# Kernel optimization log

Measured on AMD Instinct MI355X. Metric: run time of the kernel, lower is better.

The kernel has to match this reference:

```python
import jax, jax.numpy as jnp
import numpy as np

D_MODEL = 1024
SEL_DIM = 64
CONFIGS = [(4, 32), (8, 64), (16, 128)]  # (heads, dim)
B, T = 2, 2048


def setup_inputs() -> dict:
    key = jax.random.key(0)
    ks = jax.random.split(key, 20)
    s = 0.02  # init scale for stability
    inp = {
        "x": jax.random.normal(ks[0], (B, T, D_MODEL), jnp.float32),
        "sel_w1": jax.random.normal(ks[1], (SEL_DIM, D_MODEL), jnp.float32) * s,
        "sel_b1": jnp.zeros((SEL_DIM,), jnp.float32),
        "sel_w2": jax.random.normal(ks[2], (SEL_DIM, SEL_DIM), jnp.float32) * s,
        "sel_b2": jnp.zeros((SEL_DIM,), jnp.float32),
        "sel_w3": jax.random.normal(ks[3], (len(CONFIGS), SEL_DIM), jnp.float32) * s,
        "sel_b3": jnp.zeros((len(CONFIGS),), jnp.float32),
    }
    for i, (h, d) in enumerate(CONFIGS):
        inp[f"qw{i}"] = jax.random.normal(ks[4 + 3 * i], (h * d, D_MODEL), jnp.float32) * s
        inp[f"kw{i}"] = jax.random.normal(ks[5 + 3 * i], (d, D_MODEL), jnp.float32) * s
        inp[f"ww{i}"] = jax.random.normal(ks[6 + 3 * i], (h, D_MODEL), jnp.float32) * s
    return inp


def _seq_features(x):
    # x: [b,t,d]
    b, t, d = x.shape
    seq_mean = jnp.mean(x, axis=1, keepdims=True)            # [b,1,d]
    seq_std = jnp.std(x, axis=1, keepdims=True, ddof=1)      # torch.std is unbiased
    pos = (jnp.arange(t, dtype=x.dtype) / t)[None, :, None]  # [1,t,1] broadcast to [b,t,d]
    return x + seq_mean + seq_std + pos * 0.1


def _forward(x, sel_w1, sel_b1, sel_w2, sel_b2, sel_w3, sel_b3,
             qw0, kw0, ww0, qw1, kw1, ww1, qw2, kw2, ww2):
    b, t, dm = x.shape
    feats = _seq_features(x)
    h1 = jax.nn.relu(feats @ sel_w1.T + sel_b1)
    h2 = jax.nn.relu(h1 @ sel_w2.T + sel_b2)
    config_probs = jax.nn.softmax(h2 @ sel_w3.T + sel_b3, axis=-1)  # [b,t,ncfg]

    per_cfg = [(qw0, kw0, ww0), (qw1, kw1, ww1), (qw2, kw2, ww2)]
    final = jnp.zeros((b, t, t), dtype=x.dtype)
    for i, ((heads, dim), (qw, kw, ww)) in enumerate(zip(CONFIGS, per_cfg)):
        q = (x @ qw.T).reshape(b, t, heads, dim)   # [b,t,h,d]
        k = x @ kw.T                               # [b,s,d]
        w = x @ ww.T                               # [b,t,h]
        dots = jnp.einsum('bthd,bsd->bths', q, k)  # [b,t,h,s]
        score = jnp.einsum('bths,bth->bts', jax.nn.relu(dots), w)  # relu*weight, sum heads
        final = final + config_probs[:, :, i:i + 1] * score
    return final


def reference(x, sel_w1, sel_b1, sel_w2, sel_b2, sel_w3, sel_b3,
              qw0, kw0, ww0, qw1, kw1, ww1, qw2, kw2, ww2):
    return _forward(x, sel_w1, sel_b1, sel_w2, sel_b2, sel_w3, sel_b3,
                    qw0, kw0, ww0, qw1, kw1, ww1, qw2, kw2, ww2)
```

## Files before the change

### kernel.cpp

```cpp
#include <hip/hip_runtime.h>
#include <hip/hip_fp16.h>
#include <cstdint>
#include <cstddef>
#include <math.h>

#define B_ 2
#define T_ 2048
#define D_ 1024
#define M_ (B_*T_)

#define QO0 0
#define KO0 128
#define WO0 160
#define QO1 168
#define KO1 680
#define WO1 744
#define QO2 752
#define KO2 2800
#define WO2 2928
#define SELO 2944
#define LDN 3072

typedef float f32x16 __attribute__((ext_vector_type(16)));
typedef short bf16x8 __attribute__((ext_vector_type(8)));
typedef unsigned short u16;

__device__ __forceinline__ u16 f2bf(float f) {
    unsigned int u = __float_as_uint(f);
    unsigned int r = (u + 0x7fffu + ((u >> 16) & 1u)) >> 16;
    return (u16)r;
}
__device__ __forceinline__ float bf2f(u16 b) {
    return __uint_as_float(((unsigned int)b) << 16);
}

__device__ __forceinline__ void gload16(const void* g, void* l) {
    __builtin_amdgcn_global_load_lds(
        (const __attribute__((address_space(1))) unsigned int*)g,
        (__attribute__((address_space(3))) unsigned int*)l,
        16, 0, 0);
}

__device__ __forceinline__ void stage_plane(const u16* src_base, int row_stride, int k0,
                                            int rg, int lane, u16* dst) {
    int rl  = lane >> 2;
    int row = rg * 16 + rl;
    int q   = (lane & 3) ^ (rl & 3) ^ ((rl >> 2) & 3);
    const u16* s = src_base + (size_t)row * row_stride + k0 + q * 8;
    gload16(s, dst + rg * 512);
}

__global__ void stats1(const float* __restrict__ x, float* __restrict__ part,
                       float* __restrict__ part2, u16* __restrict__ Xh) {
    int d  = blockIdx.x * 256 + threadIdx.x;
    int tc = blockIdx.y;
    int b  = blockIdx.z;
    size_t base = (size_t)b * T_ * D_ + (size_t)tc * 64 * D_ + d;
    float s = 0.f, s2 = 0.f;
#pragma unroll 8
    for (int t = 0; t < 64; ++t) {
        float v = x[base + (size_t)t * D_];
        s += v; s2 += v * v;
        Xh[base + (size_t)t * D_] = f2bf(v);
    }
    part [(b * 32 + tc) * D_ + d] = s;
    part2[(b * 32 + tc) * D_ + d] = s2;
}

__global__ void stats2(const float* __restrict__ part, const float* __restrict__ part2,
                       const float* __restrict__ w1,
                       float* __restrict__ msd, float* __restrict__ s1) {
    __shared__ float msL[1024];
    __shared__ float ps[64][17];
    __shared__ float pw[64][17];
    int b = blockIdx.x, tid = threadIdx.x;
    float s = 0.f, s2 = 0.f;
#pragma unroll 8
    for (int i = 0; i < 32; ++i) {
        s  += part [(b * 32 + i) * D_ + tid];
        s2 += part2[(b * 32 + i) * D_ + tid];
    }
    float mean = s / (float)T_;
    float var  = (s2 - (float)T_ * mean * mean) / (float)(T_ - 1);
    msL[tid] = mean + sqrtf(fmaxf(var, 0.f));
    __syncthreads();
    int j = tid >> 4, cc = tid & 15;
    float am = 0.f, aw = 0.f;
    const float* wr = w1 + (size_t)j * D_ + cc * 64;
    const float* mr = msL + cc * 64;
    for (int dd = 0; dd < 64; ++dd) { float w = wr[dd]; am += mr[dd] * w; aw += w; }
    ps[j][cc] = am; pw[j][cc] = aw;
    __syncthreads();
    if (tid < 64) {
        float sm = 0.f, sw = 0.f;
        for (int i = 0; i < 16; ++i) { sm += ps[tid][i]; sw += pw[tid][i]; }
        msd[b * 64 + tid] = sm;
        if (b == 0) s1[tid] = sw;
    }
}

__global__ void split_w(const float* __restrict__ qw0, const float* __restrict__ kw0,
                        const float* __restrict__ ww0, const float* __restrict__ qw1,
                        const float* __restrict__ kw1, const float* __restrict__ ww1,
                        const float* __restrict__ qw2, const float* __restrict__ kw2,
                        const float* __restrict__ ww2, const float* __restrict__ w1s,
                        u16* __restrict__ Wh) {
    int row = blockIdx.x;
    int col = threadIdx.x * 4;
    const float* src = nullptr;
    if      (row < 128)  src = qw0 + (size_t)row * D_;
    else if (row < 160)  src = kw0 + (size_t)(row - 128) * D_;
    else if (row < 164)  src = ww0 + (size_t)(row - 160) * D_;
    else if (row < 168)  src = nullptr;
    else if (row < 680)  src = qw1 + (size_t)(row - 168) * D_;
    else if (row < 744)  src = kw1 + (size_t)(row - 680) * D_;
    else if (row < 752)  src = ww1 + (size_t)(row - 744) * D_;
    else if (row < 2800) src = qw2 + (size_t)(row - 752) * D_;
    else if (row < 2928) src = kw2 + (size_t)(row - 2800) * D_;
    else if (row < 2944) src = ww2 + (size_t)(row - 2928) * D_;
    else if (row < 3008) src = w1s + (size_t)(row - 2944) * D_;
    float4 v = src ? *(const float4*)(src + col) : make_float4(0.f, 0.f, 0.f, 0.f);
    ushort4 h;
    h.x = f2bf(v.x); h.y = f2bf(v.y); h.z = f2bf(v.z); h.w = f2bf(v.w);
    *(ushort4*)&Wh[(size_t)row * D_ + col] = h;
}

__global__ __launch_bounds__(256, 3) void proj_gemm(
    const u16* __restrict__ Xh, const u16* __restrict__ Wh, u16* __restrict__ Ph) {
    __shared__ u16 As[8192], Bs[8192];
    int tid = threadIdx.x;
    int wave = tid >> 6, lane = tid & 63;
    int bm = blockIdx.x * 128, bn = blockIdx.y * 128;
    int wt = wave >> 1, wn = wave & 1;
    int fm = lane & 31, hv = lane >> 5;
    int tkey = (fm & 3) ^ ((fm >> 2) & 3);
    f32x16 acc[2][2];
#pragma unroll
    for (int i = 0; i < 2; ++i)
#pragma unroll
        for (int j = 0; j < 2; ++j)
#pragma unroll
            for (int r = 0; r < 16; ++r) acc[i][j][r] = 0.f;

    const u16* xh = Xh + (size_t)bm * D_;
    const u16* wh = Wh + (size_t)bn * D_;

    for (int kc = 0; kc < 16; ++kc) {
        int k0 = kc * 64;
#pragma unroll
        for (int i = 0; i < 8; ++i) {
            int j = wave * 8 + i;
            int mat = j >> 4;
            int pl  = (j >> 3) & 1;
            int rg  = j & 7;
            stage_plane(mat ? wh : xh, D_, k0 + pl * 32, rg, lane,
                        (mat ? Bs : As) + pl * 4096);
        }
        __syncthreads();
#pragma unroll
        for (int ks = 0; ks < 4; ++ks) {
            int pl = ks >> 1;
            int slot8 = (((ks & 1) * 2 + hv) ^ tkey) * 8;
            bf16x8 a_h[2], b_h[2];
#pragma unroll
            for (int t = 0; t < 2; ++t) {
                a_h[t] = *(const bf16x8*)&As[pl * 4096 + (wt * 64 + t * 32 + fm) * 32 + slot8];
                b_h[t] = *(const bf16x8*)&Bs[pl * 4096 + (wn * 64 + t * 32 + fm) * 32 + slot8];
            }
#pragma unroll
            for (int ti = 0; ti < 2; ++ti)
#pragma unroll
                for (int tj = 0; tj < 2; ++tj)
                    acc[ti][tj] = __builtin_amdgcn_mfma_f32_32x32x16_bf16(a_h[ti], b_h[tj], acc[ti][tj], 0, 0, 0);
        }
        __syncthreads();
    }
#pragma unroll
    for (int ti = 0; ti < 2; ++ti)
#pragma unroll
        for (int tj = 0; tj < 2; ++tj)
#pragma unroll
            for (int r = 0; r < 16; ++r) {
                int row = bm + wt * 64 + ti * 32 + (r & 3) + 8 * (r >> 2) + 4 * hv;
                int col = bn + wn * 64 + tj * 32 + fm;
                Ph[(size_t)row * LDN + col] = f2bf(acc[ti][tj][r]);
            }
}

__global__ void selector2(const u16* __restrict__ Ph,
                          const float* __restrict__ msd, const float* __restrict__ s1,
                          const float* __restrict__ b1, const float* __restrict__ w2,
                          const float* __restrict__ b2, const float* __restrict__ w3,
                          const float* __restrict__ b3, __half* __restrict__ WP) {
    __shared__ float h1s[4][64];
    __shared__ float h2s[4][64];
    __shared__ float lg[4][3];
    int tid = threadIdx.x;
    int slot = tid >> 6, j = tid & 63;
    int bt = blockIdx.x * 4 + slot;
    int b = bt >> 11, t = bt & 2047;
    size_t pidx = (size_t)bt * LDN + SELO + j;
    float v = bf2f(Ph[pidx])
            + msd[b * 64 + j] + 0.1f * ((float)t / (float)T_) * s1[j] + b1[j];
    h1s[slot][j] = fmaxf(v, 0.f);
    __syncthreads();
    float a2 = b2[j];
#pragma unroll 8
    for (int d = 0; d < 64; ++d) a2 = fmaf(h1s[slot][d], w2[j * 64 + d], a2);
    h2s[slot][j] = fmaxf(a2, 0.f);
    __syncthreads();
    if (j < 3) {
        float a3 = b3[j];
        for (int d = 0; d < 64; ++d) a3 = fmaf(h2s[slot][d], w3[j * 64 + d], a3);
        lg[slot][j] = a3;
    }
    __syncthreads();
    if (j < 28) {
        float m = fmaxf(lg[slot][0], fmaxf(lg[slot][1], lg[slot][2]));
        float e0 = expf(lg[slot][0] - m), e1 = expf(lg[slot][1] - m), e2 = expf(lg[slot][2] - m);
        float inv = 1.f / (e0 + e1 + e2);
        int wcol = (j < 4) ? (WO0 + j) : ((j < 12) ? (WO1 + j - 4) : (WO2 + j - 12));
        float p = ((j < 4) ? e0 : ((j < 12) ? e1 : e2)) * inv;
        float w = bf2f(Ph[(size_t)bt * LDN + wcol]);
        WP[(size_t)(b * 28 + j) * T_ + t] = __float2half(w * p);
    }
}

__device__ __forceinline__ int qcol_of(int c) {
    if (c < 2)  return QO0 + c * 64;
    if (c < 10) return QO1 + (c - 2) * 64;
    return QO2 + (c - 10) * 64;
}

__global__ __launch_bounds__(256, 2) void score_kernel(
    const u16* __restrict__ Ph, const __half* __restrict__ WP, float* __restrict__ out) {
    __shared__ u16 Qs[2][8192];
    __shared__ u16 Ks[4 * 4096];
    __shared__ __half wpL[3584];
    int tid = threadIdx.x;
    int wave = tid >> 6, lane = tid & 63;
    int wt = wave >> 1, wn = wave & 1;
    int fm = lane & 31, hv = lane >> 5;
    int tkey = (fm & 3) ^ ((fm >> 2) & 3);

    int n = blockIdx.z * 256 + blockIdx.y * 16 + blockIdx.x;
    int p = (n & 7) * 4 + (n >> 7);
    int xb = (n >> 3) & 15;
    int b = p >> 4, yb = p & 15;
    int t0 = yb * 128, s0 = xb * 128;

    const u16* Pq = Ph + (size_t)(b * T_ + t0) * LDN;
    const u16* Pk = Ph + (size_t)(b * T_ + s0) * LDN;

    auto stageQ = [&](int buf, int qcol) {
#pragma unroll
        for (int i = 0; i < 4; ++i) {
            int j = (wave << 2) + i;
            int pl = j >> 3, rg = j & 7;
            stage_plane(Pq, LDN, qcol + pl * 32, rg, lane, &Qs[buf][pl * 4096]);
        }
    };

#pragma unroll
    for (int i = 0; i < 6; ++i) {
        int j = i * 4 + wave;
        int pl = j >> 3, rg = j & 7;
        int col = (pl == 0) ? KO0 : ((pl == 1) ? KO1 : KO1 + 32);
        stage_plane(Pk, LDN, col, rg, lane, &Ks[pl * 4096]);
    }
#pragma unroll
    for (int i = 0; i < 2; ++i) {
        int j = i * 4 + wave;
        if (j < 7) {
            const __half* src = WP + (size_t)(b * 28 + j * 4 + (lane >> 4)) * T_ + t0 + (lane & 15) * 8;
            gload16(src, (u16*)wpL + j * 512);
        }
    }
    stageQ(0, QO0);

    f32x16 outacc[2][2], dots[2][2], Z16;
#pragma unroll
    for (int r = 0; r < 16; ++r) Z16[r] = 0.f;
#pragma unroll
    for (int i = 0; i < 2; ++i)
#pragma unroll
        for (int j = 0; j < 2; ++j)
#pragma unroll
            for (int r = 0; r < 16; ++r) { outacc[i][j][r] = 0.f; dots[i][j][r] = 0.f; }

    auto epi = [&](int g) {
#pragma unroll
        for (int ti = 0; ti < 2; ++ti) {
            int rowbase = wt * 64 + ti * 32 + 4 * hv;
#pragma unroll
            for (int rq = 0; rq < 4; ++rq) {
                const __half2* wp2 = (const __half2*)&wpL[g * 128 + rowbase + rq * 8];
                float2 f01 = __half22float2(wp2[0]);
                float2 f23 = __half22float2(wp2[1]);
                float wv[4] = {f01.x, f01.y, f23.x, f23.y};
#pragma unroll
                for (int tj = 0; tj < 2; ++tj)
#pragma unroll
                    for (int r2 = 0; r2 < 4; ++r2) {
                        int r = rq * 4 + r2;
                        outacc[ti][tj][r] += fmaxf(dots[ti][tj][r], 0.f) * wv[r2];
                    }
            }
        }
    };

    auto runPhase = [&](int c, int kpA, int kpB, bool z0, bool midBreak,
                        int gMid, bool hasEnd, int gEnd) {
        if (c + 1 < 42) {
            stageQ((c + 1) & 1, qcol_of(c + 1));
            asm volatile("s_waitcnt vmcnt(4)" ::: "memory");
        } else {
            asm volatile("s_waitcnt vmcnt(0)" ::: "memory");
        }
        __builtin_amdgcn_s_barrier();
        __builtin_amdgcn_sched_barrier(0);
        const u16* qb = Qs[c & 1];

        bf16x8 kf[2][2], qf[2][2];
        auto loadks = [&](int ks, int sl) {
            int kp = (ks < 2) ? kpA : kpB;
            int slot8 = (((ks & 1) * 2 + hv) ^ tkey) * 8;
#pragma unroll
            for (int tj = 0; tj < 2; ++tj)
                kf[sl][tj] = *(const bf16x8*)&Ks[kp * 4096 + (wn * 64 + tj * 32 + fm) * 32 + slot8];
#pragma unroll
            for (int ti = 0; ti < 2; ++ti)
                qf[sl][ti] = *(const bf16x8*)&qb[(ks >> 1) * 4096 + (wt * 64 + ti * 32 + fm) * 32 + slot8];
        };
        loadks(0, 0);
#pragma unroll
        for (int ks = 0; ks < 4; ++ks) {
            if (ks < 3) loadks(ks + 1, (ks + 1) & 1);
            bool zero = (ks == 0 && z0) || (ks == 2 && midBreak);
            int sl = ks & 1;
            __builtin_amdgcn_s_setprio(1);
#pragma unroll
            for (int ti = 0; ti < 2; ++ti)
#pragma unroll
                for (int tj = 0; tj < 2; ++tj)
                    dots[ti][tj] = __builtin_amdgcn_mfma_f32_32x32x16_bf16(
                        qf[sl][ti], kf[sl][tj], zero ? Z16 : dots[ti][tj], 0, 0, 0);
            __builtin_amdgcn_s_setprio(0);
            if (ks == 1 && midBreak) epi(gMid);
            if (ks == 3 && hasEnd)   epi(gEnd);
        }
        __builtin_amdgcn_sched_barrier(0);
        __builtin_amdgcn_s_barrier();
    };

#pragma unroll
    for (int c = 0; c < 2; ++c)
        runPhase(c, 0, 0, true, true, 2 * c, true, 2 * c + 1);
    for (int h = 0; h < 8; ++h) {
        runPhase(2 + h, 1, 2, true, false, -1, true, 4 + h);
        if (h == 7) {
            for (int j = wave; j < 32; j += 4) {
                int pl = j >> 3, rg = j & 7;
                stage_plane(Pk, LDN, KO2 + pl * 32, rg, lane, &Ks[pl * 4096]);
            }
        }
    }
    for (int h = 0; h < 16; ++h) {
        runPhase(10 + 2 * h, 0, 1, true, false, -1, false, -1);
        runPhase(11 + 2 * h, 2, 3, false, false, -1, true, 12 + h);
    }

#pragma unroll
    for (int ti = 0; ti < 2; ++ti)
#pragma unroll
        for (int tj = 0; tj < 2; ++tj)
#pragma unroll
            for (int r = 0; r < 16; ++r) {
                int trow = wt * 64 + ti * 32 + (r & 3) + 8 * (r >> 2) + 4 * hv;
                int scol = wn * 64 + tj * 32 + fm;
                out[(size_t)(b * T_ + t0 + trow) * T_ + (s0 + scol)] = outacc[ti][tj][r];
            }
}

extern "C" void kernel_launch(void* const* d_in, const int* in_sizes, int n_in,
                              void* d_out, int out_size, void* d_ws, size_t ws_size,
                              hipStream_t stream) {
    const float* x   = (const float*)d_in[0];
    const float* w1  = (const float*)d_in[1];
    const float* b1  = (const float*)d_in[2];
    const float* w2  = (const float*)d_in[3];
    const float* b2  = (const float*)d_in[4];
    const float* w3  = (const float*)d_in[5];
    const float* b3  = (const float*)d_in[6];
    const float* qw0 = (const float*)d_in[7];
    const float* kw0 = (const float*)d_in[8];
    const float* ww0 = (const float*)d_in[9];
    const float* qw1 = (const float*)d_in[10];
    const float* kw1 = (const float*)d_in[11];
    const float* ww1 = (const float*)d_in[12];
    const float* qw2 = (const float*)d_in[13];
    const float* kw2 = (const float*)d_in[14];
    const float* ww2 = (const float*)d_in[15];
    float* out = (float*)d_out;

    float* fb = (float*)d_ws;
    float* PA  = fb; fb += (size_t)B_ * 32 * D_;
    float* PA2 = fb; fb += (size_t)B_ * 32 * D_;
    float* MSD = fb; fb += 128;
    float* S1  = fb; fb += 64;
    __half* WP = (__half*)fb; fb += (size_t)B_ * 28 * T_ / 2;
    u16* ub = (u16*)fb;
    u16* Wh = ub; ub += (size_t)LDN * D_;
    u16* Xh = ub; ub += (size_t)M_ * D_;
    u16* Ph = ub; ub += (size_t)M_ * LDN;

    stats1<<<dim3(D_ / 256, 32, B_), 256, 0, stream>>>(x, PA, PA2, Xh);
    stats2<<<dim3(B_), 1024, 0, stream>>>(PA, PA2, w1, MSD, S1);
    split_w<<<dim3(LDN), 256, 0, stream>>>(qw0, kw0, ww0, qw1, kw1, ww1,
                                           qw2, kw2, ww2, w1, Wh);
    proj_gemm<<<dim3(M_ / 128, LDN / 128), 256, 0, stream>>>(Xh, Wh, Ph);
    selector2<<<dim3(M_ / 4), 256, 0, stream>>>(Ph, MSD, S1, b1, w2, b2, w3, b3, WP);
    score_kernel<<<dim3(T_ / 128, T_ / 128, B_), 256, 0, stream>>>(Ph, WP, out);
}
```

Before: 250.6 us.

## Load Q fragments directly from global memory instead of double-buffered LDS staging

Removes the double-buffered shared-memory staging of Q tiles and the per-phase barriers. Each wave now loads its Q MFMA fragments straight from global memory (L2-resident projections) into registers, while K stays in LDS and is restaged with explicit barriers only between config groups. This cuts LDS traffic, LDS footprint and block-wide synchronisation. In exchange, global load latency sits directly in front of the MFMAs with no software prefetch, and each wave issues uncoalesced row-strided loads.

```diff
diff --git a/kernel.cpp b/kernel.cpp
--- a/kernel.cpp
+++ b/kernel.cpp
@@ -226,15 +226,8 @@
     }
 }
 
-__device__ __forceinline__ int qcol_of(int c) {
-    if (c < 2)  return QO0 + c * 64;
-    if (c < 10) return QO1 + (c - 2) * 64;
-    return QO2 + (c - 10) * 64;
-}
-
 __global__ __launch_bounds__(256, 2) void score_kernel(
     const u16* __restrict__ Ph, const __half* __restrict__ WP, float* __restrict__ out) {
-    __shared__ u16 Qs[2][8192];
     __shared__ u16 Ks[4 * 4096];
     __shared__ __half wpL[3584];
     int tid = threadIdx.x;
@@ -252,15 +245,6 @@
     const u16* Pq = Ph + (size_t)(b * T_ + t0) * LDN;
     const u16* Pk = Ph + (size_t)(b * T_ + s0) * LDN;
 
-    auto stageQ = [&](int buf, int qcol) {
-#pragma unroll
-        for (int i = 0; i < 4; ++i) {
-            int j = (wave << 2) + i;
-            int pl = j >> 3, rg = j & 7;
-            stage_plane(Pq, LDN, qcol + pl * 32, rg, lane, &Qs[buf][pl * 4096]);
-        }
-    };
-
 #pragma unroll
     for (int i = 0; i < 6; ++i) {
         int j = i * 4 + wave;
@@ -276,7 +260,9 @@
             gload16(src, (u16*)wpL + j * 512);
         }
     }
-    stageQ(0, QO0);
+    asm volatile("s_waitcnt vmcnt(0)" ::: "memory");
+    __builtin_amdgcn_s_barrier();
+    __builtin_amdgcn_sched_barrier(0);
 
     f32x16 outacc[2][2], dots[2][2], Z16;
 #pragma unroll
@@ -309,65 +295,59 @@
         }
     };
 
-    auto runPhase = [&](int c, int kpA, int kpB, bool z0, bool midBreak,
+    auto runPhase = [&](int qcol, int kpA, int kpB, bool z0, bool midBreak,
                         int gMid, bool hasEnd, int gEnd) {
-        if (c + 1 < 42) {
-            stageQ((c + 1) & 1, qcol_of(c + 1));
-            asm volatile("s_waitcnt vmcnt(4)" ::: "memory");
-        } else {
-            asm volatile("s_waitcnt vmcnt(0)" ::: "memory");
-        }
-        __builtin_amdgcn_s_barrier();
-        __builtin_amdgcn_sched_barrier(0);
-        const u16* qb = Qs[c & 1];
-
-        bf16x8 kf[2][2], qf[2][2];
-        auto loadks = [&](int ks, int sl) {
+        const u16* q0 = Pq + (size_t)(wt * 64 + fm) * LDN + qcol + hv * 8;
+        const u16* q1 = q0 + (size_t)32 * LDN;
+        bf16x8 qf[2][4];
+#pragma unroll
+        for (int ks = 0; ks < 4; ++ks) {
+            qf[0][ks] = *(const bf16x8*)(q0 + ks * 16);
+            qf[1][ks] = *(const bf16x8*)(q1 + ks * 16);
+        }
+#pragma unroll
+        for (int ks = 0; ks < 4; ++ks) {
             int kp = (ks < 2) ? kpA : kpB;
             int slot8 = (((ks & 1) * 2 + hv) ^ tkey) * 8;
+            bf16x8 kf[2];
 #pragma unroll
             for (int tj = 0; tj < 2; ++tj)
-                kf[sl][tj] = *(const bf16x8*)&Ks[kp * 4096 + (wn * 64 + tj * 32 + fm) * 32 + slot8];
-#pragma unroll
-            for (int ti = 0; ti < 2; ++ti)
-                qf[sl][ti] = *(const bf16x8*)&qb[(ks >> 1) * 4096 + (wt * 64 + ti * 32 + fm) * 32 + slot8];
-        };
-        loadks(0, 0);
-#pragma unroll
-        for (int ks = 0; ks < 4; ++ks) {
-            if (ks < 3) loadks(ks + 1, (ks + 1) & 1);
+                kf[tj] = *(const bf16x8*)&Ks[kp * 4096 + (wn * 64 + tj * 32 + fm) * 32 + slot8];
             bool zero = (ks == 0 && z0) || (ks == 2 && midBreak);
-            int sl = ks & 1;
             __builtin_amdgcn_s_setprio(1);
 #pragma unroll
             for (int ti = 0; ti < 2; ++ti)
 #pragma unroll
                 for (int tj = 0; tj < 2; ++tj)
                     dots[ti][tj] = __builtin_amdgcn_mfma_f32_32x32x16_bf16(
-                        qf[sl][ti], kf[sl][tj], zero ? Z16 : dots[ti][tj], 0, 0, 0);
+                        qf[ti][ks], kf[tj], zero ? Z16 : dots[ti][tj], 0, 0, 0);
             __builtin_amdgcn_s_setprio(0);
             if (ks == 1 && midBreak) epi(gMid);
             if (ks == 3 && hasEnd)   epi(gEnd);
         }
-        __builtin_amdgcn_sched_barrier(0);
-        __builtin_amdgcn_s_barrier();
     };
 
 #pragma unroll
     for (int c = 0; c < 2; ++c)
-        runPhase(c, 0, 0, true, true, 2 * c, true, 2 * c + 1);
-    for (int h = 0; h < 8; ++h) {
-        runPhase(2 + h, 1, 2, true, false, -1, true, 4 + h);
-        if (h == 7) {
-            for (int j = wave; j < 32; j += 4) {
-                int pl = j >> 3, rg = j & 7;
-                stage_plane(Pk, LDN, KO2 + pl * 32, rg, lane, &Ks[pl * 4096]);
-            }
-        }
-    }
+        runPhase(QO0 + c * 64, 0, 0, true, true, 2 * c, true, 2 * c + 1);
+    for (int h = 0; h < 8; ++h)
+        runPhase(QO1 + h * 64, 1, 2, true, false, -1, true, 4 + h);
+
+    __builtin_amdgcn_sched_barrier(0);
+    asm volatile("s_waitcnt lgkmcnt(0)" ::: "memory");
+    __builtin_amdgcn_s_barrier();
+    __builtin_amdgcn_sched_barrier(0);
+    for (int j = wave; j < 32; j += 4) {
+        int pl = j >> 3, rg = j & 7;
+        stage_plane(Pk, LDN, KO2 + pl * 32, rg, lane, &Ks[pl * 4096]);
+    }
+    asm volatile("s_waitcnt vmcnt(0)" ::: "memory");
+    __builtin_amdgcn_s_barrier();
+    __builtin_amdgcn_sched_barrier(0);
+
     for (int h = 0; h < 16; ++h) {
-        runPhase(10 + 2 * h, 0, 1, true, false, -1, false, -1);
-        runPhase(11 + 2 * h, 2, 3, false, false, -1, true, 12 + h);
+        runPhase(QO2 + (2 * h) * 64,     0, 1, true,  false, -1, false, -1);
+        runPhase(QO2 + (2 * h + 1) * 64, 2, 3, false, false, -1, true, 12 + h);
     }
 
 #pragma unroll
```

Result: slower. 266.7 us (+6.4%).

## Split score kernel tiles across eight waves instead of four

Applied to the files above, without the earlier changes.

The score kernel goes from 256 to 512 threads per block. Each wave now owns a 64x32 output sub-tile instead of 64x64, and staging of Q, K and WP is spread over eight waves. The K/Q fragment double-buffering is removed in favour of simple per-step loads, and an explicit wait and barrier are added after the initial staging. This is meant to raise latency hiding and occupancy through more waves with fewer accumulator registers each, at the cost of more LDS reads per MFMA and more barrier participants.

```diff
diff --git a/kernel.cpp b/kernel.cpp
--- a/kernel.cpp
+++ b/kernel.cpp
@@ -232,14 +232,14 @@
     return QO2 + (c - 10) * 64;
 }
 
-__global__ __launch_bounds__(256, 2) void score_kernel(
+__global__ __launch_bounds__(512, 4) void score_kernel(
     const u16* __restrict__ Ph, const __half* __restrict__ WP, float* __restrict__ out) {
     __shared__ u16 Qs[2][8192];
     __shared__ u16 Ks[4 * 4096];
     __shared__ __half wpL[3584];
     int tid = threadIdx.x;
     int wave = tid >> 6, lane = tid & 63;
-    int wt = wave >> 1, wn = wave & 1;
+    int wt = wave >> 2, wn = wave & 3;
     int fm = lane & 31, hv = lane >> 5;
     int tkey = (fm & 3) ^ ((fm >> 2) & 3);
 
@@ -254,39 +254,34 @@
 
     auto stageQ = [&](int buf, int qcol) {
 #pragma unroll
-        for (int i = 0; i < 4; ++i) {
-            int j = (wave << 2) + i;
+        for (int i = 0; i < 2; ++i) {
+            int j = wave * 2 + i;
             int pl = j >> 3, rg = j & 7;
             stage_plane(Pq, LDN, qcol + pl * 32, rg, lane, &Qs[buf][pl * 4096]);
         }
     };
 
 #pragma unroll
-    for (int i = 0; i < 6; ++i) {
-        int j = i * 4 + wave;
+    for (int i = 0; i < 3; ++i) {
+        int j = i * 8 + wave;
         int pl = j >> 3, rg = j & 7;
         int col = (pl == 0) ? KO0 : ((pl == 1) ? KO1 : KO1 + 32);
         stage_plane(Pk, LDN, col, rg, lane, &Ks[pl * 4096]);
     }
-#pragma unroll
-    for (int i = 0; i < 2; ++i) {
-        int j = i * 4 + wave;
-        if (j < 7) {
-            const __half* src = WP + (size_t)(b * 28 + j * 4 + (lane >> 4)) * T_ + t0 + (lane & 15) * 8;
-            gload16(src, (u16*)wpL + j * 512);
-        }
+    if (wave < 7) {
+        const __half* src = WP + (size_t)(b * 28 + wave * 4 + (lane >> 4)) * T_ + t0 + (lane & 15) * 8;
+        gload16(src, (u16*)wpL + wave * 512);
     }
     stageQ(0, QO0);
-
-    f32x16 outacc[2][2], dots[2][2], Z16;
-#pragma unroll
-    for (int r = 0; r < 16; ++r) Z16[r] = 0.f;
+    asm volatile("s_waitcnt vmcnt(0)" ::: "memory");
+    __builtin_amdgcn_s_barrier();
+    __builtin_amdgcn_sched_barrier(0);
+
+    f32x16 outacc[2], dots[2];
 #pragma unroll
     for (int i = 0; i < 2; ++i)
 #pragma unroll
-        for (int j = 0; j < 2; ++j)
-#pragma unroll
-            for (int r = 0; r < 16; ++r) { outacc[i][j][r] = 0.f; dots[i][j][r] = 0.f; }
+        for (int r = 0; r < 16; ++r) { outacc[i][r] = 0.f; dots[i][r] = 0.f; }
 
     auto epi = [&](int g) {
 #pragma unroll
@@ -299,12 +294,10 @@
                 float2 f23 = __half22float2(wp2[1]);
                 float wv[4] = {f01.x, f01.y, f23.x, f23.y};
 #pragma unroll
-                for (int tj = 0; tj < 2; ++tj)
-#pragma unroll
-                    for (int r2 = 0; r2 < 4; ++r2) {
-                        int r = rq * 4 + r2;
-                        outacc[ti][tj][r] += fmaxf(dots[ti][tj][r], 0.f) * wv[r2];
-                    }
+                for (int r2 = 0; r2 < 4; ++r2) {
+                    int r = rq * 4 + r2;
+                    outacc[ti][r] += fmaxf(dots[ti][r], 0.f) * wv[r2];
+                }
             }
         }
     };
@@ -313,7 +306,7 @@
                         int gMid, bool hasEnd, int gEnd) {
         if (c + 1 < 42) {
             stageQ((c + 1) & 1, qcol_of(c + 1));
-            asm volatile("s_waitcnt vmcnt(4)" ::: "memory");
+            asm volatile("s_waitcnt vmcnt(2)" ::: "memory");
         } else {
             asm volatile("s_waitcnt vmcnt(0)" ::: "memory");
         }
@@ -321,30 +314,27 @@
         __builtin_amdgcn_sched_barrier(0);
         const u16* qb = Qs[c & 1];
 
-        bf16x8 kf[2][2], qf[2][2];
-        auto loadks = [&](int ks, int sl) {
+#pragma unroll
+        for (int ks = 0; ks < 4; ++ks) {
             int kp = (ks < 2) ? kpA : kpB;
             int slot8 = (((ks & 1) * 2 + hv) ^ tkey) * 8;
-#pragma unroll
-            for (int tj = 0; tj < 2; ++tj)
-                kf[sl][tj] = *(const bf16x8*)&Ks[kp * 4096 + (wn * 64 + tj * 32 + fm) * 32 + slot8];
+            bf16x8 kf = *(const bf16x8*)&Ks[kp * 4096 + (wn * 32 + fm) * 32 + slot8];
+            bf16x8 qf[2];
 #pragma unroll
             for (int ti = 0; ti < 2; ++ti)
-                qf[sl][ti] = *(const bf16x8*)&qb[(ks >> 1) * 4096 + (wt * 64 + ti * 32 + fm) * 32 + slot8];
-        };
-        loadks(0, 0);
-#pragma unroll
-        for (int ks = 0; ks < 4; ++ks) {
-            if (ks < 3) loadks(ks + 1, (ks + 1) & 1);
+                qf[ti] = *(const bf16x8*)&qb[(ks >> 1) * 4096 + (wt * 64 + ti * 32 + fm) * 32 + slot8];
             bool zero = (ks == 0 && z0) || (ks == 2 && midBreak);
-            int sl = ks & 1;
+            if (zero) {
+#pragma unroll
+                for (int ti = 0; ti < 2; ++ti)
+#pragma unroll
+                    for (int r = 0; r < 16; ++r) dots[ti][r] = 0.f;
+            }
             __builtin_amdgcn_s_setprio(1);
 #pragma unroll
             for (int ti = 0; ti < 2; ++ti)
-#pragma unroll
-                for (int tj = 0; tj < 2; ++tj)
-                    dots[ti][tj] = __builtin_amdgcn_mfma_f32_32x32x16_bf16(
-                        qf[sl][ti], kf[sl][tj], zero ? Z16 : dots[ti][tj], 0, 0, 0);
+                dots[ti] = __builtin_amdgcn_mfma_f32_32x32x16_bf16(
+                    qf[ti], kf, dots[ti], 0, 0, 0);
             __builtin_amdgcn_s_setprio(0);
             if (ks == 1 && midBreak) epi(gMid);
             if (ks == 3 && hasEnd)   epi(gEnd);
@@ -359,7 +349,7 @@
     for (int h = 0; h < 8; ++h) {
         runPhase(2 + h, 1, 2, true, false, -1, true, 4 + h);
         if (h == 7) {
-            for (int j = wave; j < 32; j += 4) {
+            for (int j = wave; j < 32; j += 8) {
                 int pl = j >> 3, rg = j & 7;
                 stage_plane(Pk, LDN, KO2 + pl * 32, rg, lane, &Ks[pl * 4096]);
             }
@@ -373,13 +363,11 @@
 #pragma unroll
     for (int ti = 0; ti < 2; ++ti)
 #pragma unroll
-        for (int tj = 0; tj < 2; ++tj)
-#pragma unroll
-            for (int r = 0; r < 16; ++r) {
-                int trow = wt * 64 + ti * 32 + (r & 3) + 8 * (r >> 2) + 4 * hv;
-                int scol = wn * 64 + tj * 32 + fm;
-                out[(size_t)(b * T_ + t0 + trow) * T_ + (s0 + scol)] = outacc[ti][tj][r];
-            }
+        for (int r = 0; r < 16; ++r) {
+            int trow = wt * 64 + ti * 32 + (r & 3) + 8 * (r >> 2) + 4 * hv;
+            int scol = wn * 32 + fm;
+            out[(size_t)(b * T_ + t0 + trow) * T_ + (s0 + scol)] = outacc[ti][r];
+        }
 }
 
 extern "C" void kernel_launch(void* const* d_in, const int* in_sizes, int n_in,
@@ -420,5 +408,5 @@
                                            qw2, kw2, ww2, w1, Wh);
     proj_gemm<<<dim3(M_ / 128, LDN / 128), 256, 0, stream>>>(Xh, Wh, Ph);
     selector2<<<dim3(M_ / 4), 256, 0, stream>>>(Ph, MSD, S1, b1, w2, b2, w3, b3, WP);
-    score_kernel<<<dim3(T_ / 128, T_ / 128, B_), 256, 0, stream>>>(Ph, WP, out);
-}
+    score_kernel<<<dim3(T_ / 128, T_ / 128, B_), 512, 0, stream>>>(Ph, WP, out);
+}
```

After: 257.3 us. +2.7%, slower.
